# Kernel tuning notes

Measured on AMD Instinct MI355X. Metric: run time of the kernel, lower is better.

## Reference

```python
import jax, jax.numpy as jnp
import numpy as np

N = 100000
E = 640000
IN_CH = 64
HID = 128
HEADS = [4, 4, 1]
BN_EPS = 1e-5
NEG_SLOPE = 0.2  # GATConv default leaky relu slope


def setup_inputs() -> dict:
    key = jax.random.key(0)
    ks = iter(jax.random.split(key, 48))
    nrm = lambda shape, s=0.1: jax.random.normal(next(ks), shape, jnp.float32) * s
    return dict(
        x=jax.random.normal(next(ks), (N, IN_CH), jnp.float32),
        edge_index=jax.random.randint(next(ks), (2, E), 0, N),
        edge_weight=jax.random.uniform(next(ks), (E,), jnp.float32),
        Wproj=nrm((IN_CH, HID)), bproj=jnp.zeros((HID,), jnp.float32),
        gat_W=nrm((3, HID, HID)), att_src=nrm((3, HID)), att_dst=nrm((3, HID)),
        att_edge=nrm((3, HID)), lin_edge_W=nrm((3, HID)),
        gat_bias=jnp.zeros((3, HID), jnp.float32),
        bn_gamma=jnp.ones((3, HID), jnp.float32), bn_beta=jnp.zeros((3, HID), jnp.float32),
        bn_mean=nrm((3, HID), 0.05),
        bn_var=jax.random.uniform(next(ks), (3, HID), jnp.float32, 0.5, 1.5),
        ew_W1=nrm((3, 32)), ew_b1=jnp.zeros((3, 32), jnp.float32),
        ew_W2=nrm((3, 32)), ew_b2=jnp.zeros((3,), jnp.float32),
        symptom_attention=jnp.ones((HID,), jnp.float32),
        clf_W1=nrm((HID, 64)), clf_b1=jnp.zeros((64,), jnp.float32),
        clf_bn_gamma=jnp.ones((64,), jnp.float32), clf_bn_beta=jnp.zeros((64,), jnp.float32),
        clf_bn_mean=nrm((64,), 0.05),
        clf_bn_var=jax.random.uniform(next(ks), (64,), jnp.float32, 0.5, 1.5),
        clf_W2=nrm((64, 32)), clf_b2=jnp.zeros((32,), jnp.float32),
        clf_W3=nrm((32, 2)), clf_b3=jnp.zeros((2,), jnp.float32),
    )


def _bn(x, g, b, m, v):
    # eval-mode BatchNorm with running stats
    return (x - m) * jax.lax.rsqrt(v + BN_EPS) * g + b


def reference(x, edge_index, edge_weight, Wproj, bproj, gat_W, att_src, att_dst,
              att_edge, lin_edge_W, gat_bias, bn_gamma, bn_beta, bn_mean, bn_var,
              ew_W1, ew_b1, ew_W2, ew_b2, symptom_attention, clf_W1, clf_b1,
              clf_bn_gamma, clf_bn_beta, clf_bn_mean, clf_bn_var, clf_W2, clf_b2,
              clf_W3, clf_b3):
    n = x.shape[0]
    loop = jnp.arange(n)
    src = jnp.concatenate([edge_index[0], loop])  # [E+N] self loops appended
    dst = jnp.concatenate([edge_index[1], loop])
    h = x @ Wproj + bproj  # input projection -> [N, HID]
    for i, H in enumerate(HEADS):
        C = HID // H
        # edge attention MLP: Linear(1,32)->ReLU->Linear(32,1)->Sigmoid on raw edge_weight
        eh = jax.nn.relu(edge_weight[:, None] * ew_W1[i][None, :] + ew_b1[i])
        ea = jax.nn.sigmoid(eh @ ew_W2[i] + ew_b2[i])  # [E]
        few = edge_weight * ea  # final edge weight [E]
        # self-loop edge attr fill_value='mean'
        e_attr = jnp.concatenate([few, jnp.broadcast_to(jnp.mean(few), (n,))])  # [E+N]
        # GATConv
        xl = (h @ gat_W[i]).reshape(n, H, C)
        a_src = jnp.sum(xl * att_src[i].reshape(H, C), axis=-1)  # [N,H]
        a_dst = jnp.sum(xl * att_dst[i].reshape(H, C), axis=-1)  # [N,H]
        e_lin = (e_attr[:, None] * lin_edge_W[i][None, :]).reshape(-1, H, C)
        a_edge = jnp.sum(e_lin * att_edge[i].reshape(H, C), axis=-1)  # [E+N,H]
        alpha = jax.nn.leaky_relu(a_src[src] + a_dst[dst] + a_edge, NEG_SLOPE)
        amax = jax.ops.segment_max(alpha, dst, num_segments=n)
        ex = jnp.exp(alpha - amax[dst])
        denom = jax.ops.segment_sum(ex, dst, num_segments=n)
        w = ex / (denom[dst] + 1e-16)  # segment softmax over incoming edges
        out = jax.ops.segment_sum(w[:, :, None] * xl[src], dst, num_segments=n)
        h = out.reshape(n, HID) + gat_bias[i]
        h = jax.nn.elu(_bn(h, bn_gamma[i], bn_beta[i], bn_mean[i], bn_var[i]))
        # dropout is identity in eval mode
    h = h * symptom_attention
    c = jax.nn.relu(h @ clf_W1 + clf_b1)
    c = _bn(c, clf_bn_gamma, clf_bn_beta, clf_bn_mean, clf_bn_var)
    c = jax.nn.relu(c @ clf_W2 + clf_b2)
    logits = c @ clf_W3 + clf_b3
    return logits
```

## Files before the change

kernel.cpp:

```cpp
#include <hip/hip_runtime.h>
#include <hip/hip_fp16.h>
#include <math.h>

#define NN 100000
#define EE 640000
#define ENL (EE + NN)
#define HIDD 128

constexpr float BN_EPS = 1e-5f;

typedef _Float16 f16x8 __attribute__((ext_vector_type(8)));
typedef float f32x4 __attribute__((ext_vector_type(4)));

template<int KDIM, int NC, int EPI>
__global__ __launch_bounds__(256) void k_gemm(
    const float* __restrict__ A, const float* __restrict__ W,
    const float* __restrict__ bias, float* __restrict__ out, int nrows,
    const float* __restrict__ bng, const float* __restrict__ bnb,
    const float* __restrict__ bnm, const float* __restrict__ bnv)
{
    constexpr int TXN = NC / 4;
    constexpr int TYN = 256 / TXN;
    constexpr int RPT = 64 / TYN;
    __shared__ float Al[64][36];
    __shared__ float Wl[32][NC];
    const int t = threadIdx.x;
    const int tx = t % TXN, ty = t / TXN;
    const long rowBase = (long)blockIdx.x * 64;
    float acc[RPT][4];
#pragma unroll
    for (int r = 0; r < RPT; ++r) { acc[r][0]=0.f; acc[r][1]=0.f; acc[r][2]=0.f; acc[r][3]=0.f; }

    for (int kk = 0; kk < KDIM; kk += 32) {
#pragma unroll
        for (int j = 0; j < 2; ++j) {
            int idx = t + j * 256;
            int r = idx >> 3;
            int k4 = (idx & 7) << 2;
            long gr = rowBase + r;
            float4 v = make_float4(0.f, 0.f, 0.f, 0.f);
            if (gr < nrows) v = *(const float4*)(A + gr * KDIM + kk + k4);
            *(float4*)&Al[r][k4] = v;
        }
        constexpr int WLOAD = (32 * NC / 4) / 256;
#pragma unroll
        for (int j = 0; j < WLOAD; ++j) {
            int idx = t + j * 256;
            int k = idx / TXN;
            int c4 = (idx % TXN) << 2;
            *(float4*)&Wl[k][c4] = *(const float4*)(W + (long)(kk + k) * NC + c4);
        }
        __syncthreads();
#pragma unroll
        for (int k = 0; k < 32; ++k) {
            float4 wv = *(float4*)&Wl[k][tx * 4];
#pragma unroll
            for (int r = 0; r < RPT; ++r) {
                float av = Al[ty * RPT + r][k];
                acc[r][0] = fmaf(av, wv.x, acc[r][0]);
                acc[r][1] = fmaf(av, wv.y, acc[r][1]);
                acc[r][2] = fmaf(av, wv.z, acc[r][2]);
                acc[r][3] = fmaf(av, wv.w, acc[r][3]);
            }
        }
        __syncthreads();
    }

    const int col0 = tx * 4;
    if constexpr (EPI == 0) {
        float4 b4 = *(const float4*)(bias + col0);
#pragma unroll
        for (int r = 0; r < RPT; ++r) {
            long row = rowBase + ty * RPT + r;
            if (row < nrows) {
                float4 o = make_float4(acc[r][0] + b4.x, acc[r][1] + b4.y,
                                       acc[r][2] + b4.z, acc[r][3] + b4.w);
                *(float4*)(out + row * NC + col0) = o;
            }
        }
    } else {
        float4 b4 = *(const float4*)(bias + col0);
        float4 g4 = *(const float4*)(bng + col0);
        float4 be4 = *(const float4*)(bnb + col0);
        float4 m4 = *(const float4*)(bnm + col0);
        float4 v4 = *(const float4*)(bnv + col0);
        float s0 = rsqrtf(v4.x + BN_EPS) * g4.x;
        float s1 = rsqrtf(v4.y + BN_EPS) * g4.y;
        float s2 = rsqrtf(v4.z + BN_EPS) * g4.z;
        float s3 = rsqrtf(v4.w + BN_EPS) * g4.w;
#pragma unroll
        for (int r = 0; r < RPT; ++r) {
            long row = rowBase + ty * RPT + r;
            if (row < nrows) {
                float o0 = fmaxf(acc[r][0] + b4.x, 0.f);
                float o1 = fmaxf(acc[r][1] + b4.y, 0.f);
                float o2 = fmaxf(acc[r][2] + b4.z, 0.f);
                float o3 = fmaxf(acc[r][3] + b4.w, 0.f);
                float4 o = make_float4((o0 - m4.x) * s0 + be4.x,
                                       (o1 - m4.y) * s1 + be4.y,
                                       (o2 - m4.z) * s2 + be4.z,
                                       (o3 - m4.w) * s3 + be4.w);
                *(float4*)(out + row * NC + col0) = o;
            }
        }
    }
}

__global__ void k_prepW(const float* __restrict__ Wk, __half* __restrict__ Wt)
{
    int idx = blockIdx.x * 256 + threadIdx.x;
    int k = idx >> 7, n = idx & 127;
    Wt[n * 128 + k] = (__half)Wk[idx];
}

__global__ __launch_bounds__(256) void k_mgemm(
    const float* __restrict__ A, const __half* __restrict__ Wt,
    __half* __restrict__ xlh, int nrows)
{
    __shared__ _Float16 Ah[64][136];
    __shared__ _Float16 Wl[128][136];
    const int t = threadIdx.x;
    const int lane = t & 63, w = t >> 6;
    const long rowBase = (long)blockIdx.x * 64;

#pragma unroll
    for (int j = 0; j < 8; ++j) {
        int flat = t + j * 256;
        int r = flat >> 5;
        int c4 = (flat & 31) << 2;
        float4 v = make_float4(0.f, 0.f, 0.f, 0.f);
        long gr = rowBase + r;
        if (gr < nrows) v = *(const float4*)(A + gr * 128 + c4);
        _Float16* dst = &Ah[r][c4];
        dst[0] = (_Float16)v.x; dst[1] = (_Float16)v.y;
        dst[2] = (_Float16)v.z; dst[3] = (_Float16)v.w;
    }
#pragma unroll
    for (int j = 0; j < 8; ++j) {
        int flat = t + j * 256;
        int r = flat >> 4;
        int ch = (flat & 15) << 3;
        *(uint4*)&Wl[r][ch] = *(const uint4*)(Wt + r * 128 + ch);
    }
    __syncthreads();

    const int row16 = lane & 15, kb = lane >> 4;
    f32x4 acc[8];
#pragma unroll
    for (int cb = 0; cb < 8; ++cb) acc[cb] = (f32x4){0.f, 0.f, 0.f, 0.f};
#pragma unroll
    for (int ks = 0; ks < 4; ++ks) {
        f16x8 a = *(const f16x8*)&Ah[w * 16 + row16][ks * 32 + kb * 8];
#pragma unroll
        for (int cb = 0; cb < 8; ++cb) {
            f16x8 b = *(const f16x8*)&Wl[cb * 16 + row16][ks * 32 + kb * 8];
            acc[cb] = __builtin_amdgcn_mfma_f32_16x16x32_f16(a, b, acc[cb], 0, 0, 0);
        }
    }

    _Float16 (*Oh)[136] = Ah;
#pragma unroll
    for (int cb = 0; cb < 8; ++cb) {
#pragma unroll
        for (int r = 0; r < 4; ++r) {
            Oh[w * 16 + kb * 4 + r][cb * 16 + row16] = (_Float16)acc[cb][r];
        }
    }
    __syncthreads();
#pragma unroll
    for (int j = 0; j < 4; ++j) {
        int flat = t + j * 256;
        int r = flat >> 4;
        int ch = (flat & 15) << 3;
        long gr = rowBase + r;
        if (gr < nrows) *(uint4*)(xlh + gr * 128 + ch) = *(const uint4*)&Oh[r][ch];
    }
}

template<int H>
__global__ __launch_bounds__(256) void k_att(
    const __half* __restrict__ xlh, const float* __restrict__ att_s,
    const float* __restrict__ att_d, float* __restrict__ asrc,
    float* __restrict__ adst)
{
    int gid = blockIdx.x * 256 + threadIdx.x;
    if (gid >= NN * H) return;
    int row = gid / H, h = gid % H;
    constexpr int C = 128 / H;
    const __half* xr = xlh + (size_t)row * 128 + h * C;
    const float* as = att_s + h * C;
    const float* ad = att_d + h * C;
    float ps = 0.f, pd = 0.f;
#pragma unroll
    for (int c = 0; c < C; c += 2) {
        float2 f = __half22float2(*(const __half2*)(xr + c));
        ps = fmaf(f.x, as[c], ps); ps = fmaf(f.y, as[c + 1], ps);
        pd = fmaf(f.x, ad[c], pd); pd = fmaf(f.y, ad[c + 1], pd);
    }
    asrc[gid] = ps;
    adst[gid] = pd;
}

__global__ void k_prep(const float* __restrict__ lew, const float* __restrict__ ae,
                       float* __restrict__ scal, int H)
{
    __shared__ float p[128];
    int t = threadIdx.x;
    p[t] = lew[t] * ae[t];
    __syncthreads();
    if (t == 0) scal[0] = 0.f;
    if (t < H) {
        int Cc = 128 / H;
        float s = 0.f;
        for (int c = 0; c < Cc; ++c) s += p[t * Cc + c];
        scal[4 + t] = s;
    }
}

__global__ __launch_bounds__(256) void k_edgemlp(
    const float* __restrict__ ew, const float* __restrict__ W1,
    const float* __restrict__ b1, const float* __restrict__ W2,
    const float* __restrict__ b2, float* __restrict__ few,
    float* __restrict__ sumfew)
{
    __shared__ float red[4];
    int e = blockIdx.x * 256 + threadIdx.x;
    float f = 0.f;
    if (e < EE) {
        float w = ew[e];
        float acc = b2[0];
#pragma unroll
        for (int j = 0; j < 32; ++j) {
            float t_ = fmaf(w, W1[j], b1[j]);
            t_ = fmaxf(t_, 0.f);
            acc = fmaf(t_, W2[j], acc);
        }
        f = w / (1.f + __expf(-acc));
        few[e] = f;
    }
    float s = f;
#pragma unroll
    for (int m_ = 1; m_ < 64; m_ <<= 1) s += __shfl_xor(s, m_, 64);
    int lane = threadIdx.x & 63, wid = threadIdx.x >> 6;
    if (lane == 0) red[wid] = s;
    __syncthreads();
    if (threadIdx.x == 0) atomicAdd(sumfew, red[0] + red[1] + red[2] + red[3]);
}

__global__ __launch_bounds__(256) void k_hist(const int* __restrict__ edst, int* __restrict__ cnt)
{
    int e = blockIdx.x * 256 + threadIdx.x;
    if (e < ENL) {
        int d = (e < EE) ? edst[e] : (e - EE);
        atomicAdd(&cnt[d], 1);
    }
}

__global__ __launch_bounds__(256) void k_scan1(const int* __restrict__ cnt,
                                               int* __restrict__ tmp, int* __restrict__ part)
{
    __shared__ int s1[256];
    int t = threadIdx.x;
    int i = blockIdx.x * 256 + t;
    int x = (i < NN) ? cnt[i] : 0;
    s1[t] = x;
    __syncthreads();
#pragma unroll
    for (int off = 1; off < 256; off <<= 1) {
        int v_ = (t >= off) ? s1[t - off] : 0;
        __syncthreads();
        s1[t] += v_;
        __syncthreads();
    }
    if (i < NN) tmp[i] = s1[t] - x;
    if (t == 255) part[blockIdx.x] = s1[255];
}

__global__ void k_scan2(int* __restrict__ part, int nb)
{
    __shared__ int s1[512];
    int t = threadIdx.x;
    int x = (t < nb) ? part[t] : 0;
    s1[t] = x;
    __syncthreads();
#pragma unroll
    for (int off = 1; off < 512; off <<= 1) {
        int v_ = (t >= off) ? s1[t - off] : 0;
        __syncthreads();
        s1[t] += v_;
        __syncthreads();
    }
    if (t < nb) part[t] = s1[t] - x;
}

__global__ __launch_bounds__(256) void k_scan3(int* __restrict__ rp, int* __restrict__ cur,
                                               const int* __restrict__ part)
{
    int i = blockIdx.x * 256 + threadIdx.x;
    if (i < NN) {
        int v_ = rp[i] + part[blockIdx.x];
        rp[i] = v_;
        cur[i] = v_;
    } else if (i == NN) {
        rp[NN] = ENL;
    }
}

__global__ __launch_bounds__(256) void k_scatter(const int* __restrict__ edst,
                                                 int* __restrict__ cur, int* __restrict__ eid)
{
    int e = blockIdx.x * 256 + threadIdx.x;
    if (e < ENL) {
        int d = (e < EE) ? edst[e] : (e - EE);
        int pos = atomicAdd(&cur[d], 1);
        eid[pos] = e;
    }
}

__global__ __launch_bounds__(256) void k_psrc(const int* __restrict__ eid,
                                              const int* __restrict__ esrc,
                                              int* __restrict__ ssrc)
{
    int p = blockIdx.x * 256 + threadIdx.x;
    if (p < ENL) {
        int e = eid[p];
        ssrc[p] = (e < EE) ? esrc[e] : (e - EE);
    }
}

__global__ __launch_bounds__(256) void k_pfew(const int* __restrict__ eid,
                                              const float* __restrict__ few,
                                              const float* __restrict__ scal,
                                              float* __restrict__ sfew)
{
    int p = blockIdx.x * 256 + threadIdx.x;
    if (p < ENL) {
        int e = eid[p];
        sfew[p] = (e < EE) ? few[e] : scal[0] * (1.0f / EE);
    }
}

template<int H>
__global__ __launch_bounds__(256) void k_agg(
    const __half* __restrict__ xl, const float* __restrict__ a_src,
    const float* __restrict__ a_dst, const float* __restrict__ sfew,
    const int* __restrict__ ssrc, const float* __restrict__ scal,
    const int* __restrict__ rp,
    const float* __restrict__ bias, const float* __restrict__ bng,
    const float* __restrict__ bnb, const float* __restrict__ bnm,
    const float* __restrict__ bnv, float* __restrict__ hout)
{
    __shared__ float lw[4][H][66];
    const int lane = threadIdx.x & 63;
    const int wid  = threadIdx.x >> 6;
    const int n = (blockIdx.x << 2) + wid;
    float Kc[H], adn[H];
#pragma unroll
    for (int h = 0; h < H; ++h) { Kc[h] = scal[4 + h]; adn[h] = a_dst[n * H + h]; }
    const int p0 = rp[n];
    const int deg = rp[n + 1] - p0;
    const bool fast = (deg <= 64);

    float acc0 = 0.f, acc1 = 0.f;

    if (fast) {
        const bool act = lane < deg;
        float al[H];
        if (act) {
            int s = ssrc[p0 + lane];
            float ea = sfew[p0 + lane];
            if constexpr (H == 4) {
                float4 as = *(const float4*)(a_src + s * 4);
                float x0 = as.x + adn[0] + ea * Kc[0];
                float x1 = as.y + adn[1] + ea * Kc[1];
                float x2 = as.z + adn[2] + ea * Kc[2];
                float x3 = as.w + adn[3] + ea * Kc[3];
                al[0] = (x0 > 0.f) ? x0 : 0.2f * x0;
                al[1] = (x1 > 0.f) ? x1 : 0.2f * x1;
                al[2] = (x2 > 0.f) ? x2 : 0.2f * x2;
                al[3] = (x3 > 0.f) ? x3 : 0.2f * x3;
            } else {
                float x0 = a_src[s] + adn[0] + ea * Kc[0];
                al[0] = (x0 > 0.f) ? x0 : 0.2f * x0;
            }
        } else {
#pragma unroll
            for (int h = 0; h < H; ++h) al[h] = -INFINITY;
        }
        float mx[H], ex[H], dn[H];
#pragma unroll
        for (int h = 0; h < H; ++h) {
            mx[h] = al[h];
#pragma unroll
            for (int m_ = 1; m_ < 64; m_ <<= 1) mx[h] = fmaxf(mx[h], __shfl_xor(mx[h], m_, 64));
        }
#pragma unroll
        for (int h = 0; h < H; ++h) {
            ex[h] = act ? __expf(al[h] - mx[h]) : 0.f;
            dn[h] = ex[h];
#pragma unroll
            for (int m_ = 1; m_ < 64; m_ <<= 1) dn[h] += __shfl_xor(dn[h], m_, 64);
            lw[wid][h][lane] = ex[h] * (1.0f / (dn[h] + 1e-16f));
        }
    }
    __syncthreads();

    if (fast) {
        const int myh = (H == 4) ? (lane >> 4) : 0;
        const float* wrow = &lw[wid][myh][0];
        int j = 0;
        for (; j + 4 <= deg; j += 4) {
            int s0 = ssrc[p0 + j + 0];
            int s1 = ssrc[p0 + j + 1];
            int s2 = ssrc[p0 + j + 2];
            int s3 = ssrc[p0 + j + 3];
            float w0 = wrow[j + 0], w1 = wrow[j + 1], w2 = wrow[j + 2], w3 = wrow[j + 3];
            float2 f0 = __half22float2(((const __half2*)(xl + (size_t)s0 * HIDD))[lane]);
            float2 f1 = __half22float2(((const __half2*)(xl + (size_t)s1 * HIDD))[lane]);
            float2 f2 = __half22float2(((const __half2*)(xl + (size_t)s2 * HIDD))[lane]);
            float2 f3 = __half22float2(((const __half2*)(xl + (size_t)s3 * HIDD))[lane]);
            acc0 = fmaf(w0, f0.x, acc0); acc1 = fmaf(w0, f0.y, acc1);
            acc0 = fmaf(w1, f1.x, acc0); acc1 = fmaf(w1, f1.y, acc1);
            acc0 = fmaf(w2, f2.x, acc0); acc1 = fmaf(w2, f2.y, acc1);
            acc0 = fmaf(w3, f3.x, acc0); acc1 = fmaf(w3, f3.y, acc1);
        }
        for (; j < deg; ++j) {
            int s0 = ssrc[p0 + j];
            float w0 = wrow[j];
            float2 f0 = __half22float2(((const __half2*)(xl + (size_t)s0 * HIDD))[lane]);
            acc0 = fmaf(w0, f0.x, acc0); acc1 = fmaf(w0, f0.y, acc1);
        }
    } else {
        float mx[H], dn[H];
#pragma unroll
        for (int h = 0; h < H; ++h) mx[h] = -INFINITY;
        for (int base = 0; base < deg; base += 64) {
            int j = base + lane;
            if (j < deg) {
                int s = ssrc[p0 + j];
                float ea = sfew[p0 + j];
#pragma unroll
                for (int h = 0; h < H; ++h) {
                    float x_ = a_src[s * H + h] + adn[h] + ea * Kc[h];
                    x_ = (x_ > 0.f) ? x_ : 0.2f * x_;
                    mx[h] = fmaxf(mx[h], x_);
                }
            }
        }
#pragma unroll
        for (int h = 0; h < H; ++h) {
#pragma unroll
            for (int m_ = 1; m_ < 64; m_ <<= 1) mx[h] = fmaxf(mx[h], __shfl_xor(mx[h], m_, 64));
            dn[h] = 0.f;
        }
        for (int base = 0; base < deg; base += 64) {
            int j = base + lane;
            if (j < deg) {
                int s = ssrc[p0 + j];
                float ea = sfew[p0 + j];
#pragma unroll
                for (int h = 0; h < H; ++h) {
                    float x_ = a_src[s * H + h] + adn[h] + ea * Kc[h];
                    x_ = (x_ > 0.f) ? x_ : 0.2f * x_;
                    dn[h] += __expf(x_ - mx[h]);
                }
            }
        }
#pragma unroll
        for (int h = 0; h < H; ++h) {
#pragma unroll
            for (int m_ = 1; m_ < 64; m_ <<= 1) dn[h] += __shfl_xor(dn[h], m_, 64);
            dn[h] = 1.0f / (dn[h] + 1e-16f);
        }
        for (int j = 0; j < deg; ++j) {
            int s = ssrc[p0 + j];
            float ea = sfew[p0 + j];
            float wsel;
            if constexpr (H == 4) {
                float4 as = *(const float4*)(a_src + s * 4);
                float x0 = as.x + adn[0] + ea * Kc[0]; x0 = (x0 > 0.f) ? x0 : 0.2f * x0;
                float x1 = as.y + adn[1] + ea * Kc[1]; x1 = (x1 > 0.f) ? x1 : 0.2f * x1;
                float x2 = as.z + adn[2] + ea * Kc[2]; x2 = (x2 > 0.f) ? x2 : 0.2f * x2;
                float x3 = as.w + adn[3] + ea * Kc[3]; x3 = (x3 > 0.f) ? x3 : 0.2f * x3;
                float w0 = __expf(x0 - mx[0]) * dn[0];
                float w1 = __expf(x1 - mx[1]) * dn[1];
                float w2 = __expf(x2 - mx[2]) * dn[2];
                float w3 = __expf(x3 - mx[3]) * dn[3];
                wsel = (lane < 16) ? w0 : ((lane < 32) ? w1 : ((lane < 48) ? w2 : w3));
            } else {
                float x0 = a_src[s] + adn[0] + ea * Kc[0]; x0 = (x0 > 0.f) ? x0 : 0.2f * x0;
                wsel = __expf(x0 - mx[0]) * dn[0];
            }
            float2 f = __half22float2(((const __half2*)(xl + (size_t)s * HIDD))[lane]);
            acc0 = fmaf(wsel, f.x, acc0);
            acc1 = fmaf(wsel, f.y, acc1);
        }
    }

    {
        int c0 = 2 * lane;
        float2 bi = *(const float2*)(bias + c0);
        float2 g  = *(const float2*)(bng + c0);
        float2 bb = *(const float2*)(bnb + c0);
        float2 mm = *(const float2*)(bnm + c0);
        float2 vv = *(const float2*)(bnv + c0);
        float o0 = acc0 + bi.x;
        o0 = (o0 - mm.x) * rsqrtf(vv.x + BN_EPS) * g.x + bb.x;
        o0 = (o0 > 0.f) ? o0 : (__expf(o0) - 1.f);
        float o1 = acc1 + bi.y;
        o1 = (o1 - mm.y) * rsqrtf(vv.y + BN_EPS) * g.y + bb.y;
        o1 = (o1 > 0.f) ? o1 : (__expf(o1) - 1.f);
        *(float2*)(hout + (size_t)n * HIDD + c0) = make_float2(o0, o1);
    }
}

__global__ void k_scaleW1(const float* __restrict__ W1, const float* __restrict__ sym,
                          float* __restrict__ W1s)
{
    int i = blockIdx.x * 256 + threadIdx.x;
    if (i < 128 * 64) W1s[i] = W1[i] * sym[i >> 6];
}

__global__ __launch_bounds__(256) void k_clf2(const float* __restrict__ c1,
                                              const float* __restrict__ W2,
                                              const float* __restrict__ b2,
                                              float* __restrict__ c2)
{
    __shared__ float Wl[64][32];
    int t = threadIdx.x;
#pragma unroll
    for (int j = 0; j < 2; ++j) {
        int idx = t + j * 256;
        ((float4*)Wl)[idx] = ((const float4*)W2)[idx];
    }
    __syncthreads();
    int n = blockIdx.x * 256 + t;
    if (n >= NN) return;
    float acc[32];
#pragma unroll
    for (int j = 0; j < 32; ++j) acc[j] = b2[j];
    const float* row = c1 + (long)n * 64;
#pragma unroll
    for (int k0 = 0; k0 < 64; k0 += 4) {
        float4 hv = *(const float4*)(row + k0);
#pragma unroll
        for (int kk = 0; kk < 4; ++kk) {
            float h_ = (&hv.x)[kk];
#pragma unroll
            for (int j4 = 0; j4 < 8; ++j4) {
                float4 w4 = *(float4*)&Wl[k0 + kk][j4 * 4];
                acc[j4 * 4 + 0] = fmaf(h_, w4.x, acc[j4 * 4 + 0]);
                acc[j4 * 4 + 1] = fmaf(h_, w4.y, acc[j4 * 4 + 1]);
                acc[j4 * 4 + 2] = fmaf(h_, w4.z, acc[j4 * 4 + 2]);
                acc[j4 * 4 + 3] = fmaf(h_, w4.w, acc[j4 * 4 + 3]);
            }
        }
    }
    float* o = c2 + (long)n * 32;
#pragma unroll
    for (int j4 = 0; j4 < 8; ++j4) {
        float4 v = make_float4(fmaxf(acc[j4 * 4 + 0], 0.f), fmaxf(acc[j4 * 4 + 1], 0.f),
                               fmaxf(acc[j4 * 4 + 2], 0.f), fmaxf(acc[j4 * 4 + 3], 0.f));
        *(float4*)(o + j4 * 4) = v;
    }
}

__global__ __launch_bounds__(256) void k_clf3(const float* __restrict__ c2,
                                              const float* __restrict__ W3,
                                              const float* __restrict__ b3,
                                              float* __restrict__ out)
{
    int n = blockIdx.x * 256 + threadIdx.x;
    if (n >= NN) return;
    const float* row = c2 + (long)n * 32;
    float l0 = b3[0], l1 = b3[1];
#pragma unroll
    for (int k = 0; k < 32; ++k) {
        float cv = row[k];
        l0 = fmaf(cv, W3[k * 2 + 0], l0);
        l1 = fmaf(cv, W3[k * 2 + 1], l1);
    }
    *(float2*)(out + (long)n * 2) = make_float2(l0, l1);
}

extern "C" void kernel_launch(void* const* d_in, const int* in_sizes, int n_in,
                              void* d_out, int out_size, void* d_ws, size_t ws_size,
                              hipStream_t stream)
{
    const float* x          = (const float*)d_in[0];
    const int*   edge_index = (const int*)d_in[1];
    const float* edge_w     = (const float*)d_in[2];
    const float* Wproj      = (const float*)d_in[3];
    const float* bproj      = (const float*)d_in[4];
    const float* gat_W      = (const float*)d_in[5];
    const float* att_src    = (const float*)d_in[6];
    const float* att_dst    = (const float*)d_in[7];
    const float* att_edge   = (const float*)d_in[8];
    const float* lin_edge_W = (const float*)d_in[9];
    const float* gat_bias   = (const float*)d_in[10];
    const float* bn_g       = (const float*)d_in[11];
    const float* bn_b       = (const float*)d_in[12];
    const float* bn_m       = (const float*)d_in[13];
    const float* bn_v       = (const float*)d_in[14];
    const float* ew_W1      = (const float*)d_in[15];
    const float* ew_b1      = (const float*)d_in[16];
    const float* ew_W2      = (const float*)d_in[17];
    const float* ew_b2      = (const float*)d_in[18];
    const float* sym        = (const float*)d_in[19];
    const float* clf_W1     = (const float*)d_in[20];
    const float* clf_b1     = (const float*)d_in[21];
    const float* clf_bng    = (const float*)d_in[22];
    const float* clf_bnb    = (const float*)d_in[23];
    const float* clf_bnm    = (const float*)d_in[24];
    const float* clf_bnv    = (const float*)d_in[25];
    const float* clf_W2     = (const float*)d_in[26];
    const float* clf_b2     = (const float*)d_in[27];
    const float* clf_W3     = (const float*)d_in[28];
    const float* clf_b3     = (const float*)d_in[29];
    float* outp = (float*)d_out;

    float* ws   = (float*)d_ws;
    float* hbuf = ws;
    float* xlf  = hbuf + 12800000;
    __half* xl  = (__half*)xlf;
    float* c1   = xlf;
    int*   ssrc = (int*)(xlf + 6400000);
    float* sfew = xlf + 7200000;
    float* c2   = xlf + 6400000;
    float* asrc = xlf + 12800000;
    float* adst = asrc + 400000;
    float* fewp = adst + 400000;
    float* scal = fewp + 640000;
    float* W1s  = scal + 16;
    __half* Wt_h = (__half*)(W1s + 8192);
    int* rp   = (int*)(W1s + 8192 + 8192);
    int* cur  = rp + 100004;
    int* eid  = cur + 100000;
    int* part = eid + 740000;

    const int* esrc = edge_index;
    const int* edst = edge_index + EE;

    hipMemsetAsync(cur, 0, NN * sizeof(int), stream);

    k_gemm<64, 128, 0><<<1563, 256, 0, stream>>>(
        x, Wproj, bproj, hbuf, NN, nullptr, nullptr, nullptr, nullptr);

    k_hist<<<2891, 256, 0, stream>>>(edst, cur);
    k_scan1<<<391, 256, 0, stream>>>(cur, rp, part);
    k_scan2<<<1, 512, 0, stream>>>(part, 391);
    k_scan3<<<391, 256, 0, stream>>>(rp, cur, part);
    k_scatter<<<2891, 256, 0, stream>>>(edst, cur, eid);
    k_psrc<<<2891, 256, 0, stream>>>(eid, esrc, ssrc);

    for (int i = 0; i < 3; ++i) {
        int H = (i == 2) ? 1 : 4;
        k_prep<<<1, 128, 0, stream>>>(lin_edge_W + i * 128, att_edge + i * 128, scal, H);
        k_edgemlp<<<2500, 256, 0, stream>>>(edge_w, ew_W1 + i * 32, ew_b1 + i * 32,
                                            ew_W2 + i * 32, ew_b2 + i, fewp, scal);
        k_pfew<<<2891, 256, 0, stream>>>(eid, fewp, scal, sfew);
        k_prepW<<<64, 256, 0, stream>>>(gat_W + i * 128 * 128, Wt_h);
        k_mgemm<<<1563, 256, 0, stream>>>(hbuf, Wt_h, xl, NN);
        if (H == 4) {
            k_att<4><<<1563, 256, 0, stream>>>(xl, att_src + i * 128, att_dst + i * 128,
                                               asrc, adst);
            k_agg<4><<<25000, 256, 0, stream>>>(
                xl, asrc, adst, sfew, ssrc, scal, rp,
                gat_bias + i * 128, bn_g + i * 128, bn_b + i * 128,
                bn_m + i * 128, bn_v + i * 128, hbuf);
        } else {
            k_att<1><<<391, 256, 0, stream>>>(xl, att_src + i * 128, att_dst + i * 128,
                                              asrc, adst);
            k_agg<1><<<25000, 256, 0, stream>>>(
                xl, asrc, adst, sfew, ssrc, scal, rp,
                gat_bias + i * 128, bn_g + i * 128, bn_b + i * 128,
                bn_m + i * 128, bn_v + i * 128, hbuf);
        }
    }

    k_scaleW1<<<32, 256, 0, stream>>>(clf_W1, sym, W1s);
    k_gemm<128, 64, 2><<<1563, 256, 0, stream>>>(
        hbuf, W1s, clf_b1, c1, NN, clf_bng, clf_bnb, clf_bnm, clf_bnv);
    k_clf2<<<391, 256, 0, stream>>>(c1, clf_W2, clf_b2, c2);
    k_clf3<<<391, 256, 0, stream>>>(c2, clf_W3, clf_b3, outp);
}
```

Baseline: 737.6 us.

## Fuse attention dot-products into GEMM epilogue, merge prep kernels, shrink softmax shuffles

```diff
diff --git a/kernel.cpp b/kernel.cpp
--- a/kernel.cpp
+++ b/kernel.cpp
@@ -106,16 +106,34 @@
     }
 }
 
-__global__ void k_prepW(const float* __restrict__ Wk, __half* __restrict__ Wt)
-{
+__global__ void k_prepW(const float* __restrict__ Wk, __half* __restrict__ Wt,
+                        const float* __restrict__ lew, const float* __restrict__ ae,
+                        float* __restrict__ scal, int H)
+{
+    __shared__ float p[128];
     int idx = blockIdx.x * 256 + threadIdx.x;
     int k = idx >> 7, n = idx & 127;
     Wt[n * 128 + k] = (__half)Wk[idx];
-}
-
+    if (blockIdx.x == 0) {
+        int t = threadIdx.x;
+        if (t < 128) p[t] = lew[t] * ae[t];
+        __syncthreads();
+        if (t == 0) scal[0] = 0.f;
+        if (t < H) {
+            int Cc = 128 / H;
+            float s = 0.f;
+            for (int c = 0; c < Cc; ++c) s += p[t * Cc + c];
+            scal[4 + t] = s;
+        }
+    }
+}
+
+template<int H>
 __global__ __launch_bounds__(256) void k_mgemm(
     const float* __restrict__ A, const __half* __restrict__ Wt,
-    __half* __restrict__ xlh, int nrows)
+    const float* __restrict__ att_s, const float* __restrict__ att_d,
+    __half* __restrict__ xlh, float* __restrict__ asrc,
+    float* __restrict__ adst, int nrows)
 {
     __shared__ _Float16 Ah[64][136];
     __shared__ _Float16 Wl[128][136];
@@ -175,45 +193,36 @@
         long gr = rowBase + r;
         if (gr < nrows) *(uint4*)(xlh + gr * 128 + ch) = *(const uint4*)&Oh[r][ch];
     }
-}
-
-template<int H>
-__global__ __launch_bounds__(256) void k_att(
-    const __half* __restrict__ xlh, const float* __restrict__ att_s,
-    const float* __restrict__ att_d, float* __restrict__ asrc,
-    float* __restrict__ adst)
-{
-    int gid = blockIdx.x * 256 + threadIdx.x;
-    if (gid >= NN * H) return;
-    int row = gid / H, h = gid % H;
-    constexpr int C = 128 / H;
-    const __half* xr = xlh + (size_t)row * 128 + h * C;
-    const float* as = att_s + h * C;
-    const float* ad = att_d + h * C;
-    float ps = 0.f, pd = 0.f;
-#pragma unroll
-    for (int c = 0; c < C; c += 2) {
-        float2 f = __half22float2(*(const __half2*)(xr + c));
-        ps = fmaf(f.x, as[c], ps); ps = fmaf(f.y, as[c + 1], ps);
-        pd = fmaf(f.x, ad[c], pd); pd = fmaf(f.y, ad[c + 1], pd);
-    }
-    asrc[gid] = ps;
-    adst[gid] = pd;
-}
-
-__global__ void k_prep(const float* __restrict__ lew, const float* __restrict__ ae,
-                       float* __restrict__ scal, int H)
-{
-    __shared__ float p[128];
-    int t = threadIdx.x;
-    p[t] = lew[t] * ae[t];
-    __syncthreads();
-    if (t == 0) scal[0] = 0.f;
-    if (t < H) {
-        int Cc = 128 / H;
-        float s = 0.f;
-        for (int c = 0; c < Cc; ++c) s += p[t * Cc + c];
-        scal[4 + t] = s;
+
+    if constexpr (H == 4) {
+        int row = t >> 2, h = t & 3;
+        long gr = rowBase + row;
+        const float* as = att_s + h * 32;
+        const float* ad = att_d + h * 32;
+        float ps = 0.f, pd = 0.f;
+#pragma unroll
+        for (int c = 0; c < 32; c += 2) {
+            float f0 = (float)Oh[row][h * 32 + c];
+            float f1 = (float)Oh[row][h * 32 + c + 1];
+            ps = fmaf(f0, as[c], ps); ps = fmaf(f1, as[c + 1], ps);
+            pd = fmaf(f0, ad[c], pd); pd = fmaf(f1, ad[c + 1], pd);
+        }
+        if (gr < nrows) { asrc[gr * 4 + h] = ps; adst[gr * 4 + h] = pd; }
+    } else {
+        int row = t >> 2, q = t & 3;
+        long gr = rowBase + row;
+        const float* as = att_s + q * 32;
+        const float* ad = att_d + q * 32;
+        float ps = 0.f, pd = 0.f;
+#pragma unroll
+        for (int c = 0; c < 32; ++c) {
+            float f0 = (float)Oh[row][q * 32 + c];
+            ps = fmaf(f0, as[c], ps);
+            pd = fmaf(f0, ad[c], pd);
+        }
+        ps += __shfl_xor(ps, 1, 64); ps += __shfl_xor(ps, 2, 64);
+        pd += __shfl_xor(pd, 1, 64); pd += __shfl_xor(pd, 2, 64);
+        if (q == 0 && gr < nrows) { asrc[gr] = ps; adst[gr] = pd; }
     }
 }
 
@@ -365,6 +374,7 @@
 
     if (fast) {
         const bool act = lane < deg;
+        const int Wd = (deg <= 8) ? 8 : (deg <= 16) ? 16 : (deg <= 32) ? 32 : 64;
         float al[H];
         if (act) {
             int s = ssrc[p0 + lane];
@@ -391,15 +401,13 @@
 #pragma unroll
         for (int h = 0; h < H; ++h) {
             mx[h] = al[h];
-#pragma unroll
-            for (int m_ = 1; m_ < 64; m_ <<= 1) mx[h] = fmaxf(mx[h], __shfl_xor(mx[h], m_, 64));
+            for (int m_ = 1; m_ < Wd; m_ <<= 1) mx[h] = fmaxf(mx[h], __shfl_xor(mx[h], m_, 64));
         }
 #pragma unroll
         for (int h = 0; h < H; ++h) {
             ex[h] = act ? __expf(al[h] - mx[h]) : 0.f;
             dn[h] = ex[h];
-#pragma unroll
-            for (int m_ = 1; m_ < 64; m_ <<= 1) dn[h] += __shfl_xor(dn[h], m_, 64);
+            for (int m_ = 1; m_ < Wd; m_ <<= 1) dn[h] += __shfl_xor(dn[h], m_, 64);
             lw[wid][h][lane] = ex[h] * (1.0f / (dn[h] + 1e-16f));
         }
     }
@@ -655,22 +663,22 @@
 
     for (int i = 0; i < 3; ++i) {
         int H = (i == 2) ? 1 : 4;
-        k_prep<<<1, 128, 0, stream>>>(lin_edge_W + i * 128, att_edge + i * 128, scal, H);
+        k_prepW<<<64, 256, 0, stream>>>(gat_W + i * 128 * 128, Wt_h,
+                                        lin_edge_W + i * 128, att_edge + i * 128,
+                                        scal, H);
         k_edgemlp<<<2500, 256, 0, stream>>>(edge_w, ew_W1 + i * 32, ew_b1 + i * 32,
                                             ew_W2 + i * 32, ew_b2 + i, fewp, scal);
         k_pfew<<<2891, 256, 0, stream>>>(eid, fewp, scal, sfew);
-        k_prepW<<<64, 256, 0, stream>>>(gat_W + i * 128 * 128, Wt_h);
-        k_mgemm<<<1563, 256, 0, stream>>>(hbuf, Wt_h, xl, NN);
         if (H == 4) {
-            k_att<4><<<1563, 256, 0, stream>>>(xl, att_src + i * 128, att_dst + i * 128,
-                                               asrc, adst);
+            k_mgemm<4><<<1563, 256, 0, stream>>>(hbuf, Wt_h, att_src + i * 128,
+                                                 att_dst + i * 128, xl, asrc, adst, NN);
             k_agg<4><<<25000, 256, 0, stream>>>(
                 xl, asrc, adst, sfew, ssrc, scal, rp,
                 gat_bias + i * 128, bn_g + i * 128, bn_b + i * 128,
                 bn_m + i * 128, bn_v + i * 128, hbuf);
         } else {
-            k_att<1><<<391, 256, 0, stream>>>(xl, att_src + i * 128, att_dst + i * 128,
-                                              asrc, adst);
+            k_mgemm<1><<<1563, 256, 0, stream>>>(hbuf, Wt_h, att_src + i * 128,
+                                                 att_dst + i * 128, xl, asrc, adst, NN);
             k_agg<1><<<25000, 256, 0, stream>>>(
                 xl, asrc, adst, sfew, ssrc, scal, rp,
                 gat_bias + i * 128, bn_g + i * 128, bn_b + i * 128,
```

New measurement: 753.5 us. +2.2%, slower.
